# Performance work log

Hardware: AMD Instinct MI355X
Metric: run time of the kernel (lower is better)

Reference implementation:

```python
import jax, jax.numpy as jnp
import numpy as np

P = 9  # patch_size


def setup_inputs() -> dict:
    key = jax.random.key(0)
    k1, k2, k3, k4 = jax.random.split(key, 4)
    B, Cin, D, H, W = 1, 128, 36, 72, 72
    Cout = 128
    L = (D // P) * ((H * W) // P)  # 2304 non-overlapping patches
    x = jax.random.normal(k1, (B, Cin, D, H, W), dtype=jnp.float32)
    attentions = jax.random.normal(k2, (B, Cout, L, P * P), dtype=jnp.float32)
    Wc = jax.random.normal(k3, (Cout, Cin), dtype=jnp.float32) * 0.05  # conv_img 1x1x1 weight
    b = jax.random.normal(k4, (Cout,), dtype=jnp.float32) * 0.05
    return {"x": x, "attentions": attentions, "W": Wc, "b": b}


def reference(x, attentions, W, b):
    # conv_img: 1x1x1 Conv3d == per-voxel channel GEMM
    y = jnp.einsum('oc,bcdhw->bodhw', W, x) + b[None, :, None, None, None]
    B, C, D, H, Wd = y.shape
    HW = H * Wd
    y2 = y.reshape(1, C, D, HW)  # [1, C, D, H*W] as in the torch reshape
    nD, nW = D // P, HW // P
    # Unfold with kernel=stride=P (non-overlapping) == block reshape.
    # Column order: patches row-major; row order: kernel positions row-major.
    patches = (y2.reshape(1, C, nD, P, nW, P)
                 .transpose(0, 1, 2, 4, 3, 5)
                 .reshape(1, C, nD * nW, P * P))  # [1, C, L, P*P]
    nz = jnp.count_nonzero(attentions, axis=-1).astype(y2.dtype)[..., None] + 1e-5
    att = patches + attentions / nz  # [1, C, L, P*P]
    # Fold (non-overlapping) == inverse block reshape; no overlap accumulation.
    corr = (att.reshape(1, C, nD, nW, P, P)
               .transpose(0, 1, 2, 4, 3, 5)
               .reshape(1, C, D, HW))
    out = corr * y2 + y2
    return jnp.where(out >= 0, out, 0.2 * out)  # LeakyReLU(0.2)
```

## Files before the change

### kernel.cpp

```cpp
#include <hip/hip_runtime.h>
#include <hip/hip_bf16.h>

#define CIN   128
#define COUT  128
#define DD    36
#define HW    5184
#define DHW   186624
#define PATCH 9
#define NPW   576
#define L_TOT 2304
#define PP    81
#define LDSK  136

typedef __attribute__((ext_vector_type(8))) short bf16x8;
typedef __attribute__((ext_vector_type(4))) float f32x4;

__device__ __forceinline__ short f2bf(float f) {
    unsigned u = __builtin_bit_cast(unsigned, f);
    unsigned r = (u + 0x7fffu + ((u >> 16) & 1u)) >> 16;
    return (short)r;
}

__global__ __launch_bounds__(256) void count_nz(
    const float* __restrict__ attn, float* __restrict__ inv)
{
    const int pair = blockIdx.x * 256 + threadIdx.x;
    const float* ap = attn + (size_t)pair * PP;
    int cnt = 0;
    #pragma unroll
    for (int q = 0; q < PP; ++q) cnt += (ap[q] != 0.0f) ? 1 : 0;
    inv[pair] = 1.0f / ((float)cnt + 1e-5f);
}

__global__ __launch_bounds__(256) void fused_main(
    const float* __restrict__ x,
    const float* __restrict__ attn,
    const float* __restrict__ W,
    const float* __restrict__ bia,
    const float* __restrict__ inv,
    float* __restrict__ out)
{
    __shared__ __align__(16) short xs[64][LDSK];

    const int t    = threadIdx.x;
    const int wv   = t >> 6;
    const int lane = t & 63;
    const int col  = lane & 15;
    const int quad = lane >> 4;

    const int hwblk  = blockIdx.x % 81;
    const int d      = blockIdx.x / 81;
    const int hwbase = hwblk * 64;
    const int lbase  = (d / 9) * NPW;
    const int ii     = d % 9;

    #pragma unroll
    for (int e = t; e < 2048; e += 256) {
        const int row = e >> 4;
        const int f4  = e & 15;
        const float4 v = *(const float4*)(x + (size_t)row * DHW + (size_t)d * HW
                                          + hwbase + f4 * 4);
        const int n0 = f4 * 4;
        xs[n0 + 0][row] = f2bf(v.x);
        xs[n0 + 1][row] = f2bf(v.y);
        xs[n0 + 2][row] = f2bf(v.z);
        xs[n0 + 3][row] = f2bf(v.w);
    }

    const int wbase = wv * 32;
    bf16x8 afrag[2][4];
    #pragma unroll
    for (int mt = 0; mt < 2; ++mt) {
        const int m = wbase + mt * 16 + col;
        #pragma unroll
        for (int s = 0; s < 4; ++s) {
            const float4* wp4 = (const float4*)(W + m * 128 + s * 32 + quad * 8);
            float4 w0 = wp4[0], w1 = wp4[1];
            bf16x8 f;
            f[0] = f2bf(w0.x); f[1] = f2bf(w0.y); f[2] = f2bf(w0.z); f[3] = f2bf(w0.w);
            f[4] = f2bf(w1.x); f[5] = f2bf(w1.y); f[6] = f2bf(w1.z); f[7] = f2bf(w1.w);
            afrag[mt][s] = f;
        }
    }
    float bias[2][4];
    #pragma unroll
    for (int mt = 0; mt < 2; ++mt)
        #pragma unroll
        for (int r = 0; r < 4; ++r)
            bias[mt][r] = bia[wbase + mt * 16 + quad * 4 + r];

    __syncthreads();

    f32x4 acc[2][4];
    #pragma unroll
    for (int mt = 0; mt < 2; ++mt)
        #pragma unroll
        for (int tt = 0; tt < 4; ++tt)
            acc[mt][tt] = (f32x4){0.f, 0.f, 0.f, 0.f};

    #pragma unroll
    for (int s = 0; s < 4; ++s) {
        bf16x8 bfrag[4];
        #pragma unroll
        for (int tt = 0; tt < 4; ++tt)
            bfrag[tt] = *(const bf16x8*)&xs[tt * 16 + col][s * 32 + quad * 8];
        #pragma unroll
        for (int mt = 0; mt < 2; ++mt)
            #pragma unroll
            for (int tt = 0; tt < 4; ++tt)
                acc[mt][tt] = __builtin_amdgcn_mfma_f32_16x16x32_bf16(
                    afrag[mt][s], bfrag[tt], acc[mt][tt], 0, 0, 0);
    }

    #pragma unroll
    for (int tt = 0; tt < 4; ++tt) {
        const int n  = tt * 16 + col;
        const int hw = hwbase + n;
        const int p  = hw / 9;
        const int jj = hw - p * 9;
        const int l  = lbase + p;
        const int kk = ii * 9 + jj;
        #pragma unroll
        for (int mt = 0; mt < 2; ++mt) {
            #pragma unroll
            for (int r = 0; r < 4; ++r) {
                const int c = wbase + mt * 16 + quad * 4 + r;
                const float y  = acc[mt][tt][r] + bias[mt][r];
                const float a  = attn[(size_t)c * DHW + (size_t)l * PP + kk];
                const float iv = inv[c * L_TOT + l];
                const float v  = y * (y + a * iv + 1.0f);
                out[(size_t)c * DHW + (size_t)d * HW + hw] =
                    (v >= 0.f) ? v : 0.2f * v;
            }
        }
    }
}

__global__ __launch_bounds__(256) void fused_cross_head_fallback(
    const float* __restrict__ x, const float* __restrict__ attn,
    const float* __restrict__ W, const float* __restrict__ bia,
    float* __restrict__ out)
{
    __shared__ __align__(16) short xs[2][48][LDSK];
    __shared__ float inv_lds[COUT][4];

    const int t = threadIdx.x, wv = t >> 6, lane = t & 63;
    const int col = lane & 15, quad = lane >> 4;
    const int blk = blockIdx.x;
    const int pd = blk / 144, hwblk = blk - pd * 144;
    const int hwbase = hwblk * 36;
    const int lbase = pd * NPW + hwblk * 4;

    for (int pair = t; pair < 512; pair += 256) {
        const int c = pair >> 2, p = pair & 3;
        const float* ap = attn + (size_t)c * DHW + (size_t)(lbase + p) * PP;
        int cnt = 0;
        #pragma unroll 27
        for (int q = 0; q < PP; ++q) cnt += (ap[q] != 0.0f) ? 1 : 0;
        inv_lds[c][p] = 1.0f / ((float)cnt + 1e-5f);
    }
    const int wbase = wv * 32;
    bf16x8 afrag[2][4];
    #pragma unroll
    for (int mt = 0; mt < 2; ++mt) {
        const int m = wbase + mt * 16 + col;
        #pragma unroll
        for (int s = 0; s < 4; ++s) {
            const float4* wp4 = (const float4*)(W + m * 128 + s * 32 + quad * 8);
            float4 w0 = wp4[0], w1 = wp4[1];
            bf16x8 f;
            f[0] = f2bf(w0.x); f[1] = f2bf(w0.y); f[2] = f2bf(w0.z); f[3] = f2bf(w0.w);
            f[4] = f2bf(w1.x); f[5] = f2bf(w1.y); f[6] = f2bf(w1.z); f[7] = f2bf(w1.w);
            afrag[mt][s] = f;
        }
    }
    float bias[2][4];
    #pragma unroll
    for (int mt = 0; mt < 2; ++mt)
        #pragma unroll
        for (int r = 0; r < 4; ++r)
            bias[mt][r] = bia[wbase + mt * 16 + quad * 4 + r];

    for (int i = 0; i < 9; ++i) {
        const int buf = i & 1;
        const int d = pd * PATCH + i;
        for (int e = t; e < 1152; e += 256) {
            const int row = e / 9, f4 = e - row * 9;
            const float4 v = *(const float4*)(x + (size_t)row * DHW + (size_t)d * HW
                                              + hwbase + f4 * 4);
            const int n0 = f4 * 4;
            xs[buf][n0 + 0][row] = f2bf(v.x);
            xs[buf][n0 + 1][row] = f2bf(v.y);
            xs[buf][n0 + 2][row] = f2bf(v.z);
            xs[buf][n0 + 3][row] = f2bf(v.w);
        }
        __syncthreads();
        f32x4 acc[2][3];
        #pragma unroll
        for (int mt = 0; mt < 2; ++mt)
            #pragma unroll
            for (int tt = 0; tt < 3; ++tt)
                acc[mt][tt] = (f32x4){0.f, 0.f, 0.f, 0.f};
        #pragma unroll
        for (int s = 0; s < 4; ++s) {
            bf16x8 bfrag[3];
            #pragma unroll
            for (int tt = 0; tt < 3; ++tt)
                bfrag[tt] = *(const bf16x8*)&xs[buf][tt * 16 + col][s * 32 + quad * 8];
            #pragma unroll
            for (int mt = 0; mt < 2; ++mt)
                #pragma unroll
                for (int tt = 0; tt < 3; ++tt)
                    acc[mt][tt] = __builtin_amdgcn_mfma_f32_16x16x32_bf16(
                        afrag[mt][s], bfrag[tt], acc[mt][tt], 0, 0, 0);
        }
        #pragma unroll
        for (int tt = 0; tt < 3; ++tt) {
            const int n = tt * 16 + col;
            if (n < 36) {
                const int p = n / 9, jj = n - p * 9, kk = i * 9 + jj;
                #pragma unroll
                for (int mt = 0; mt < 2; ++mt) {
                    #pragma unroll
                    for (int r = 0; r < 4; ++r) {
                        const int c = wbase + mt * 16 + quad * 4 + r;
                        const float y = acc[mt][tt][r] + bias[mt][r];
                        const float a = attn[(size_t)c * DHW + (size_t)(lbase + p) * PP + kk];
                        const float v = y * (y + a * inv_lds[c][p] + 1.0f);
                        out[(size_t)c * DHW + (size_t)d * HW + hwbase + n] =
                            (v >= 0.f) ? v : 0.2f * v;
                    }
                }
            }
        }
    }
}

extern "C" void kernel_launch(void* const* d_in, const int* in_sizes, int n_in,
                              void* d_out, int out_size, void* d_ws, size_t ws_size,
                              hipStream_t stream) {
    const float* x    = (const float*)d_in[0];
    const float* attn = (const float*)d_in[1];
    const float* W    = (const float*)d_in[2];
    const float* b    = (const float*)d_in[3];
    float* out        = (float*)d_out;

    const size_t inv_bytes = (size_t)COUT * L_TOT * sizeof(float);
    if (ws_size >= inv_bytes) {
        float* inv = (float*)d_ws;
        count_nz<<<dim3((COUT * L_TOT) / 256), dim3(256), 0, stream>>>(attn, inv);
        fused_main<<<dim3(36 * 81), dim3(256), 0, stream>>>(x, attn, W, b, inv, out);
    } else {
        fused_cross_head_fallback<<<dim3(576), dim3(256), 0, stream>>>(x, attn, W, b, out);
    }
}
```

Measured before the change: 314.4 us.

## Stage attention rows in LDS as bf16 and reorder blocks for locality

count_nz now reads each block's attention rows with coalesced float4 loads, packs nonzero flags into bytes in shared memory, and then counts per row. fused_main reorders the block index so that blocks sharing an attention row are adjacent, and preloads the 9-element attention segments and inverse counts for its 8 patches into shared memory, stored as bf16. The epilogue then reads attention from LDS instead of doing scattered global gathers. Storing attention in bf16 loses precision in the correction term, and the extra LDS use may limit occupancy despite the launch-bounds hint.

```diff
diff --git a/kernel.cpp b/kernel.cpp
--- a/kernel.cpp
+++ b/kernel.cpp
@@ -20,19 +20,39 @@
     unsigned r = (u + 0x7fffu + ((u >> 16) & 1u)) >> 16;
     return (short)r;
 }
+__device__ __forceinline__ float bf2f(short s) {
+    unsigned u = ((unsigned)(unsigned short)s) << 16;
+    return __builtin_bit_cast(float, u);
+}
 
 __global__ __launch_bounds__(256) void count_nz(
     const float* __restrict__ attn, float* __restrict__ inv)
 {
-    const int pair = blockIdx.x * 256 + threadIdx.x;
-    const float* ap = attn + (size_t)pair * PP;
+    __shared__ unsigned int pred[5184];
+    const int t = threadIdx.x;
+    const float4* g = (const float4*)(attn + (size_t)blockIdx.x * 20736);
+    #pragma unroll
+    for (int k = 0; k < 20; ++k) {
+        const int idx = k * 256 + t;
+        const float4 v = g[idx];
+        pred[idx] = (v.x != 0.f ? 1u : 0u) | (v.y != 0.f ? 0x100u : 0u)
+                  | (v.z != 0.f ? 0x10000u : 0u) | (v.w != 0.f ? 0x1000000u : 0u);
+    }
+    if (t < 64) {
+        const int idx = 5120 + t;
+        const float4 v = g[idx];
+        pred[idx] = (v.x != 0.f ? 1u : 0u) | (v.y != 0.f ? 0x100u : 0u)
+                  | (v.z != 0.f ? 0x10000u : 0u) | (v.w != 0.f ? 0x1000000u : 0u);
+    }
+    __syncthreads();
+    const unsigned char* pb = (const unsigned char*)pred + t * PP;
     int cnt = 0;
     #pragma unroll
-    for (int q = 0; q < PP; ++q) cnt += (ap[q] != 0.0f) ? 1 : 0;
-    inv[pair] = 1.0f / ((float)cnt + 1e-5f);
-}
-
-__global__ __launch_bounds__(256) void fused_main(
+    for (int q = 0; q < PP; ++q) cnt += pb[q];
+    inv[(size_t)blockIdx.x * 256 + t] = 1.0f / ((float)cnt + 1e-5f);
+}
+
+__global__ __launch_bounds__(256, 4) void fused_main(
     const float* __restrict__ x,
     const float* __restrict__ attn,
     const float* __restrict__ W,
@@ -41,6 +61,8 @@
     float* __restrict__ out)
 {
     __shared__ __align__(16) short xs[64][LDSK];
+    __shared__ short sa[1024 * 9];
+    __shared__ float invs[1024];
 
     const int t    = threadIdx.x;
     const int wv   = t >> 6;
@@ -48,11 +70,25 @@
     const int col  = lane & 15;
     const int quad = lane >> 4;
 
-    const int hwblk  = blockIdx.x % 81;
-    const int d      = blockIdx.x / 81;
+    const int ii     = blockIdx.x % 9;
+    const int rest   = blockIdx.x / 9;
+    const int hwblk  = rest % 81;
+    const int pd     = rest / 81;
+    const int d      = pd * 9 + ii;
     const int hwbase = hwblk * 64;
-    const int lbase  = (d / 9) * NPW;
-    const int ii     = d % 9;
+    const int p0     = hwbase / 9;
+    const int l0     = pd * NPW + p0;
+
+    #pragma unroll
+    for (int k = 0; k < 4; ++k) {
+        const int pr = k * 256 + t;
+        const int c  = pr >> 3, lp = pr & 7;
+        const float* ap = attn + (size_t)c * DHW + (size_t)(l0 + lp) * PP + ii * 9;
+        invs[pr] = inv[c * L_TOT + l0 + lp];
+        #pragma unroll
+        for (int q = 0; q < 9; ++q)
+            sa[pr * 9 + q] = f2bf(ap[q]);
+    }
 
     #pragma unroll
     for (int e = t; e < 2048; e += 256) {
@@ -114,21 +150,19 @@
 
     #pragma unroll
     for (int tt = 0; tt < 4; ++tt) {
-        const int n  = tt * 16 + col;
-        const int hw = hwbase + n;
+        const int hw = hwbase + tt * 16 + col;
         const int p  = hw / 9;
         const int jj = hw - p * 9;
-        const int l  = lbase + p;
-        const int kk = ii * 9 + jj;
+        const int lp = p - p0;
         #pragma unroll
         for (int mt = 0; mt < 2; ++mt) {
             #pragma unroll
             for (int r = 0; r < 4; ++r) {
-                const int c = wbase + mt * 16 + quad * 4 + r;
-                const float y  = acc[mt][tt][r] + bias[mt][r];
-                const float a  = attn[(size_t)c * DHW + (size_t)l * PP + kk];
-                const float iv = inv[c * L_TOT + l];
-                const float v  = y * (y + a * iv + 1.0f);
+                const int c  = wbase + mt * 16 + quad * 4 + r;
+                const int pr = c * 8 + lp;
+                const float y = acc[mt][tt][r] + bias[mt][r];
+                const float a = bf2f(sa[pr * 9 + jj]);
+                const float v = y * (y + a * invs[pr] + 1.0f);
                 out[(size_t)c * DHW + (size_t)d * HW + hw] =
                     (v >= 0.f) ? v : 0.2f * v;
             }
```

New measurement: 338.9 us. 1.08x slower.
